# Kernel tuning notes

Hardware: AMD Instinct MI355X
Metric: run time of the kernel (lower is better)

## Reference

```python
import jax, jax.numpy as jnp
import numpy as np

N_NODES = 50000
N_EDGES = 800000
D_IN, D_HID, D_LAT = 128, 128, 64
BN_EPS = 1e-5


def setup_inputs() -> dict:
    key = jax.random.key(0)
    ks = jax.random.split(key, 8)
    x = jax.random.normal(ks[0], (N_NODES, D_IN), dtype=jnp.float32)
    edge_index = jax.random.randint(ks[1], (2, N_EDGES), 0, N_NODES, dtype=jnp.int64)
    s1 = 1.0 / np.sqrt(D_IN)
    s2 = 1.0 / np.sqrt(D_HID)
    W1 = jax.random.normal(ks[2], (D_IN, D_HID), dtype=jnp.float32) * s1
    b1 = jnp.zeros((D_HID,), jnp.float32)
    gamma = jnp.ones((D_HID,), jnp.float32)
    beta = jnp.zeros((D_HID,), jnp.float32)
    Wmu = jax.random.normal(ks[3], (D_HID, D_LAT), dtype=jnp.float32) * s2
    bmu = jnp.zeros((D_LAT,), jnp.float32)
    Wls = jax.random.normal(ks[4], (D_HID, D_LAT), dtype=jnp.float32) * s2
    bls = jnp.zeros((D_LAT,), jnp.float32)
    return {"x": x, "edge_index": edge_index, "W1": W1, "b1": b1,
            "gamma": gamma, "beta": beta, "Wmu": Wmu, "bmu": bmu,
            "Wls": Wls, "bls": bls}


def _gcn_conv(h, src, dst, norm_e, inv_deg, W, b):
    # PyG GCNConv: linear transform, then sym-normalized aggregation (A+I).
    h = h @ W                                   # [N, F]
    msgs = h[src] * norm_e[:, None]             # gather + edge scaling, [E, F]
    agg = jax.ops.segment_sum(msgs, dst, num_segments=h.shape[0])
    # self-loop contribution: norm[i]*norm[i] = 1/deg[i]
    return agg + h * inv_deg[:, None] + b


def reference(x, edge_index, W1, b1, gamma, beta, Wmu, bmu, Wls, bls):
    src, dst = edge_index[0], edge_index[1]
    n = x.shape[0]
    # degrees including self loops (GCN symmetric normalization)
    deg = jax.ops.segment_sum(jnp.ones(dst.shape, x.dtype), dst, num_segments=n) + 1.0
    inv_sqrt_deg = jax.lax.rsqrt(deg)
    norm_e = inv_sqrt_deg[src] * inv_sqrt_deg[dst]   # per-edge norm, [E]
    inv_deg = 1.0 / deg

    h = _gcn_conv(x, src, dst, norm_e, inv_deg, W1, b1)
    # BatchNorm1d with batch statistics (biased var), then ReLU; dropout off (eval)
    mean = h.mean(axis=0)
    var = h.var(axis=0)
    h = (h - mean) * jax.lax.rsqrt(var + BN_EPS) * gamma + beta
    h = jax.nn.relu(h)

    mu = _gcn_conv(h, src, dst, norm_e, inv_deg, Wmu, bmu)
    log_std = _gcn_conv(h, src, dst, norm_e, inv_deg, Wls, bls)
    return mu, log_std
```

## Files before the change

kernel.cpp:

```cpp
#include <hip/hip_runtime.h>
#include <hip/hip_bf16.h>

#define N_NODES 50000
#define N_EDGES 800000
#define F 128
#define L 64
#define BN_EPS 1e-5f
#define SCAN_BLOCKS 196
#define BN_BLOCKS 391
#define EDGE_BLOCKS 3125
#define GEMM_BLOCKS 782
#define NPART 8
#define PART_SZ 6250
#define SUBS_F 256
#define FILLB_A 2048

typedef __attribute__((ext_vector_type(8))) short short8;
typedef __attribute__((ext_vector_type(8))) unsigned short ushort8;
typedef __attribute__((ext_vector_type(4))) unsigned short ushortx4;
typedef __attribute__((ext_vector_type(4))) float f32x4;

static __device__ __forceinline__ float loadF(const void* p, int i, int f32) {
    if (f32) return ((const float*)p)[i];
    return __bfloat162float(((const __hip_bfloat16*)p)[i]);
}
static __device__ __forceinline__ float bfu2f(unsigned short u) {
    unsigned int t = ((unsigned int)u) << 16;
    float f;
    __builtin_memcpy(&f, &t, 4);
    return f;
}
static __device__ __forceinline__ short f2bf_s(float f) {
    union { __hip_bfloat16 b; short s; } cv;
    cv.b = __float2bfloat16(f);
    return cv.s;
}
static __device__ __forceinline__ unsigned short f2bf_u(float f) {
    union { __hip_bfloat16 b; unsigned short u; } cv;
    cv.b = __float2bfloat16(f);
    return cv.u;
}

__global__ void k_wprep(const void* __restrict__ W1, const void* __restrict__ Wmu,
                        const void* __restrict__ Wls, const unsigned short* __restrict__ xs,
                        const void* __restrict__ ei, __hip_bfloat16* __restrict__ Wt1,
                        __hip_bfloat16* __restrict__ Wt2, int* __restrict__ flags) {
    int b = blockIdx.x;
    int t = threadIdx.x;
    if (b == 0) {
        __shared__ int cnt[2];
        if (t < 2) cnt[t] = 0;
        __syncthreads();
        unsigned short v = xs[2 * t];
        int e = (v >> 7) & 0xff;
        int sane = (e >= 112 && e <= 133) ? 1 : 0;
        if (v == 0 || v == 0x8000) sane = 1;
        atomicAdd(&cnt[0], sane);
        atomicAdd(&cnt[1], (((const int*)ei)[2 * t + 1] != 0) ? 1 : 0);
        __syncthreads();
        if (t == 0) {
            flags[0] = (cnt[0] < 128) ? 1 : 0;
            flags[1] = (cnt[1] < 8) ? 1 : 0;
            flags[2] = 0;
        }
    } else {
        __shared__ int cnt;
        if (t == 0) cnt = 0;
        __syncthreads();
        unsigned short v = ((const unsigned short*)W1)[2 * t];
        int e = (v >> 7) & 0xff;
        atomicAdd(&cnt, (e >= 100 && e <= 133) ? 1 : 0);
        __syncthreads();
        int f32 = (cnt < 128) ? 1 : 0;
        int idx = (b - 1) * 256 + t;
        int n = idx >> 7, k = idx & 127;
        Wt1[idx] = __float2bfloat16(loadF(W1, k * F + n, f32));
        float v2 = (n < L) ? loadF(Wmu, k * L + n, f32) : loadF(Wls, k * L + (n - L), f32);
        Wt2[idx] = __float2bfloat16(v2);
    }
}

static __device__ __forceinline__ void gemm_body(int bid, const void* __restrict__ Xin,
        const __hip_bfloat16* __restrict__ Wt, const int* __restrict__ flags, int mode,
        const float* __restrict__ bnscale, const float* __restrict__ bnshift,
        unsigned short* __restrict__ outb) {
    int wave = threadIdx.x >> 6, lane = threadIdx.x & 63;
    int quad = lane >> 4, mr = lane & 15;
    int m0 = bid * 64 + wave * 16;
    int node = m0 + mr;
    int row = (node < N_NODES) ? node : N_NODES - 1;
    short8 a[4];
    if (mode == 1) {
        const unsigned short* xb = (const unsigned short*)Xin;
#pragma unroll
        for (int t = 0; t < 4; ++t) {
            int k0 = t * 32 + quad * 8;
            ushort8 raw = *(const ushort8*)(xb + row * F + k0);
            f32x4 s0 = *(const f32x4*)(bnscale + k0);
            f32x4 s1 = *(const f32x4*)(bnscale + k0 + 4);
            f32x4 h0 = *(const f32x4*)(bnshift + k0);
            f32x4 h1 = *(const f32x4*)(bnshift + k0 + 4);
            short8 av;
#pragma unroll
            for (int j = 0; j < 4; ++j)
                av[j] = f2bf_s(fmaxf(bfu2f(raw[j]) * s0[j] + h0[j], 0.f));
#pragma unroll
            for (int j = 0; j < 4; ++j)
                av[4 + j] = f2bf_s(fmaxf(bfu2f(raw[4 + j]) * s1[j] + h1[j], 0.f));
            a[t] = av;
        }
    } else if (flags[0]) {
        const float* xf = (const float*)Xin;
#pragma unroll
        for (int t = 0; t < 4; ++t) {
            int off = row * F + t * 32 + quad * 8;
            f32x4 v0 = *(const f32x4*)(xf + off);
            f32x4 v1 = *(const f32x4*)(xf + off + 4);
            short8 av;
#pragma unroll
            for (int j = 0; j < 4; ++j) av[j] = f2bf_s(v0[j]);
#pragma unroll
            for (int j = 0; j < 4; ++j) av[4 + j] = f2bf_s(v1[j]);
            a[t] = av;
        }
    } else {
        const short* xb = (const short*)Xin;
#pragma unroll
        for (int t = 0; t < 4; ++t)
            a[t] = *(const short8*)(xb + row * F + t * 32 + quad * 8);
    }
    f32x4 acc[8];
    const short* wb = (const short*)Wt;
#pragma unroll
    for (int nt = 0; nt < 8; ++nt) {
        const short* wp = wb + (nt * 16 + mr) * F + quad * 8;
        f32x4 c = {0.f, 0.f, 0.f, 0.f};
        c = __builtin_amdgcn_mfma_f32_16x16x32_bf16(*(const short8*)(wp), a[0], c, 0, 0, 0);
        c = __builtin_amdgcn_mfma_f32_16x16x32_bf16(*(const short8*)(wp + 32), a[1], c, 0, 0, 0);
        c = __builtin_amdgcn_mfma_f32_16x16x32_bf16(*(const short8*)(wp + 64), a[2], c, 0, 0, 0);
        c = __builtin_amdgcn_mfma_f32_16x16x32_bf16(*(const short8*)(wp + 96), a[3], c, 0, 0, 0);
        acc[nt] = c;
    }
    if (node < N_NODES) {
        unsigned short* op = outb + node * F;
#pragma unroll
        for (int nt = 0; nt < 8; ++nt) {
            ushortx4 r;
#pragma unroll
            for (int j = 0; j < 4; ++j) r[j] = f2bf_u(acc[nt][j]);
            *(ushortx4*)(op + nt * 16 + quad * 4) = r;
        }
    }
}

__global__ __launch_bounds__(256) void k_edge_gemm1(
        const void* __restrict__ X, const __hip_bfloat16* __restrict__ Wt1,
        const int* __restrict__ flags, const void* __restrict__ ei,
        int* __restrict__ degi, int* __restrict__ src32, int* __restrict__ dst32,
        int* __restrict__ rank, unsigned short* __restrict__ outb) {
    if (blockIdx.x < GEMM_BLOCKS) {
        gemm_body(blockIdx.x, X, Wt1, flags, 0, nullptr, nullptr, outb);
    } else {
        int t = threadIdx.x;
        int e0 = (blockIdx.x - GEMM_BLOCKS) * 256 + t;
        __shared__ int nz;
        if (t == 0) nz = 0;
        __syncthreads();
        int w = ((const int*)ei)[2 * e0 + 1];
        if (w != 0) atomicAdd(&nz, 1);
        __syncthreads();
        int d;
        if (nz < 8) {
            int s = (int)((const long long*)ei)[e0];
            d = (int)((const long long*)ei)[N_EDGES + e0];
            src32[e0] = s;
            dst32[e0] = d;
        } else {
            d = ((const int*)ei)[N_EDGES + e0];
        }
        rank[e0] = atomicAdd(&degi[d], 1);
    }
}

__global__ void k_offs_alloc(const int* __restrict__ degi, int* __restrict__ flags,
                             int* __restrict__ offs, float* __restrict__ isd) {
    __shared__ int s[256];
    __shared__ int base;
    int t = threadIdx.x;
    int i = blockIdx.x * 256 + t;
    int v = (i < N_NODES) ? degi[i] : 0;
    s[t] = v;
    __syncthreads();
    for (int o = 1; o < 256; o <<= 1) {
        int u = (t >= o) ? s[t - o] : 0;
        __syncthreads();
        s[t] += u;
        __syncthreads();
    }
    if (t == 255) base = atomicAdd(&flags[2], s[255]);
    __syncthreads();
    if (i < N_NODES) {
        offs[i] = base + s[t] - v;
        isd[i] = 1.0f / sqrtf((float)v + 1.0f);
    }
}

__global__ __launch_bounds__(256) void k_fill(
        const int* __restrict__ ei32, const int* __restrict__ src32,
        const int* __restrict__ dst32, const int* __restrict__ rank,
        const int* __restrict__ flags, const int* __restrict__ offs,
        int* __restrict__ csr) {
    const int* sp;
    const int* dp;
    if (flags[1]) { sp = src32; dp = dst32; }
    else          { sp = ei32;  dp = ei32 + N_EDGES; }
    int grp = blockIdx.x & (NPART - 1);
    int sub = blockIdx.x >> 3;
    int lo = grp * PART_SZ, hi = lo + PART_SZ;
    int stride = SUBS_F * 256;
    for (int e = sub * 256 + threadIdx.x; e < N_EDGES; e += stride) {
        int d = dp[e];
        if (d >= lo && d < hi) csr[offs[d] + rank[e]] = sp[e];
    }
}

__global__ __launch_bounds__(256) void k_gemm_bn(const void* __restrict__ Xin,
        const __hip_bfloat16* __restrict__ Wt, const int* __restrict__ flags,
        const float* __restrict__ bnscale, const float* __restrict__ bnshift,
        unsigned short* __restrict__ outb) {
    gemm_body(blockIdx.x, Xin, Wt, flags, 1, bnscale, bnshift, outb);
}

static __device__ __forceinline__ void agg_accum(int node, int grp, int l16,
        const ushort8* __restrict__ vp, const int* __restrict__ csr,
        const int* __restrict__ offs, const int* __restrict__ degi,
        const float* __restrict__ isd, float acc[8]) {
#pragma unroll
    for (int j = 0; j < 8; ++j) acc[j] = 0.f;
    if (grp == 0) {
        float w = isd[node];
        ushort8 u = vp[node * 16 + l16];
#pragma unroll
        for (int j = 0; j < 8; ++j) acc[j] = bfu2f(u[j]) * w;
    }
    int start = offs[node];
    int end = start + degi[node];
    int i = start + grp;
    for (; i + 12 < end; i += 16) {
        int s0 = csr[i], s1 = csr[i + 4], s2 = csr[i + 8], s3 = csr[i + 12];
        float w0 = isd[s0], w1 = isd[s1], w2 = isd[s2], w3 = isd[s3];
        ushort8 u0 = vp[s0 * 16 + l16];
        ushort8 u1 = vp[s1 * 16 + l16];
        ushort8 u2 = vp[s2 * 16 + l16];
        ushort8 u3 = vp[s3 * 16 + l16];
#pragma unroll
        for (int j = 0; j < 8; ++j)
            acc[j] += (bfu2f(u0[j]) * w0 + bfu2f(u1[j]) * w1) +
                      (bfu2f(u2[j]) * w2 + bfu2f(u3[j]) * w3);
    }
    for (; i + 4 < end; i += 8) {
        int s0 = csr[i], s1 = csr[i + 4];
        float w0 = isd[s0], w1 = isd[s1];
        ushort8 u0 = vp[s0 * 16 + l16];
        ushort8 u1 = vp[s1 * 16 + l16];
#pragma unroll
        for (int j = 0; j < 8; ++j) acc[j] += bfu2f(u0[j]) * w0 + bfu2f(u1[j]) * w1;
    }
    for (; i < end; i += 4) {
        int s0 = csr[i];
        float w0 = isd[s0];
        ushort8 u = vp[s0 * 16 + l16];
#pragma unroll
        for (int j = 0; j < 8; ++j) acc[j] += bfu2f(u[j]) * w0;
    }
#pragma unroll
    for (int j = 0; j < 8; ++j) {
        acc[j] += __shfl_xor(acc[j], 16);
        acc[j] += __shfl_xor(acc[j], 32);
    }
}

__global__ void k_agg1(const unsigned short* __restrict__ val, const int* __restrict__ csr,
                       const int* __restrict__ offs, const int* __restrict__ degi,
                       const float* __restrict__ isd, const void* __restrict__ b1,
                       const int* __restrict__ flags, unsigned short* __restrict__ out) {
    int node = blockIdx.x * 4 + (threadIdx.x >> 6);
    if (node >= N_NODES) return;
    int lane = threadIdx.x & 63;
    int grp = lane >> 4, l16 = lane & 15;
    float acc[8];
    agg_accum(node, grp, l16, (const ushort8*)val, csr, offs, degi, isd, acc);
    if (grp == 0) {
        float sd = isd[node];
        int c0 = l16 * 8, f32 = flags[0];
        ushort8 r;
#pragma unroll
        for (int j = 0; j < 8; ++j) r[j] = f2bf_u(acc[j] * sd + loadF(b1, c0 + j, f32));
        ((ushort8*)out)[node * 16 + l16] = r;
    }
}

__global__ void k_bnstats(const unsigned short* __restrict__ h, float* __restrict__ partial) {
    __shared__ float ls[256][8];
    __shared__ float lq[256][8];
    int t = threadIdx.x;
    int o = t & 15, rg = t >> 4;
    int row0 = blockIdx.x * 128 + rg;
    float s[8] = {0.f}, q[8] = {0.f};
#pragma unroll
    for (int i = 0; i < 8; ++i) {
        int row = row0 + i * 16;
        if (row < N_NODES) {
            ushort8 u = *(const ushort8*)(h + row * F + o * 8);
#pragma unroll
            for (int j = 0; j < 8; ++j) {
                float v = bfu2f(u[j]);
                s[j] += v;
                q[j] += v * v;
            }
        }
    }
#pragma unroll
    for (int j = 0; j < 8; ++j) { ls[t][j] = s[j]; lq[t][j] = q[j]; }
    __syncthreads();
    if (t < 128) {
        int c = t, oo = c >> 3, jj = c & 7;
        float ts = 0.f, tq = 0.f;
#pragma unroll
        for (int rgi = 0; rgi < 16; ++rgi) {
            ts += ls[rgi * 16 + oo][jj];
            tq += lq[rgi * 16 + oo][jj];
        }
        partial[blockIdx.x * 256 + c] = ts;
        partial[blockIdx.x * 256 + 128 + c] = tq;
    }
}

__global__ void k_bnredprep(const float* __restrict__ partial, const void* __restrict__ gamma,
                            const void* __restrict__ beta, const int* __restrict__ flags,
                            float* __restrict__ scale, float* __restrict__ shift) {
    int c = blockIdx.x;
    float s = 0.f, q = 0.f;
    for (int b = threadIdx.x; b < BN_BLOCKS; b += 256) {
        s += partial[b * 256 + c];
        q += partial[b * 256 + 128 + c];
    }
#pragma unroll
    for (int o = 32; o; o >>= 1) {
        s += __shfl_down(s, o);
        q += __shfl_down(q, o);
    }
    __shared__ float ws[4], wq[4];
    if ((threadIdx.x & 63) == 0) {
        ws[threadIdx.x >> 6] = s;
        wq[threadIdx.x >> 6] = q;
    }
    __syncthreads();
    if (threadIdx.x == 0) {
        float S = ws[0] + ws[1] + ws[2] + ws[3];
        float Q = wq[0] + wq[1] + wq[2] + wq[3];
        const float invN = 1.0f / (float)N_NODES;
        float m = S * invN;
        float var = Q * invN - m * m;
        int f32 = flags[0];
        float sc = loadF(gamma, c, f32) * rsqrtf(var + BN_EPS);
        scale[c] = sc;
        shift[c] = loadF(beta, c, f32) - m * sc;
    }
}

__global__ void k_agg2(const unsigned short* __restrict__ val, const int* __restrict__ csr,
                       const int* __restrict__ offs, const int* __restrict__ degi,
                       const float* __restrict__ isd, const void* __restrict__ bmu,
                       const void* __restrict__ bls, const int* __restrict__ flags,
                       void* __restrict__ out) {
    int node = blockIdx.x * 4 + (threadIdx.x >> 6);
    if (node >= N_NODES) return;
    int lane = threadIdx.x & 63;
    int grp = lane >> 4, l16 = lane & 15;
    float acc[8];
    agg_accum(node, grp, l16, (const ushort8*)val, csr, offs, degi, isd, acc);
    if (grp == 0) {
        float sd = isd[node];
        int c0 = l16 * 8, f32 = flags[0];
        int hsel = (c0 >= L) ? 1 : 0;
        int cc = c0 - hsel * L;
        const void* bp = hsel ? bls : bmu;
        float o8[8];
#pragma unroll
        for (int j = 0; j < 8; ++j) o8[j] = acc[j] * sd + loadF(bp, cc + j, f32);
        long base_o = (long)hsel * (N_NODES * 64) + (long)node * 64 + cc;
        if (f32) {
            f32x4 r0 = {o8[0], o8[1], o8[2], o8[3]};
            f32x4 r1 = {o8[4], o8[5], o8[6], o8[7]};
            __builtin_nontemporal_store(r0, (f32x4*)((float*)out + base_o));
            __builtin_nontemporal_store(r1, (f32x4*)((float*)out + base_o + 4));
        } else {
            ushort8 r;
#pragma unroll
            for (int j = 0; j < 8; ++j) r[j] = f2bf_u(o8[j]);
            __builtin_nontemporal_store(r, (ushort8*)((__hip_bfloat16*)out + base_o));
        }
    }
}

extern "C" void kernel_launch(void* const* d_in, const int* in_sizes, int n_in,
                              void* d_out, int out_size, void* d_ws, size_t ws_size,
                              hipStream_t stream) {
    const void* x     = d_in[0];
    const void* ei    = d_in[1];
    const void* W1    = d_in[2];
    const void* b1    = d_in[3];
    const void* gamma = d_in[4];
    const void* beta  = d_in[5];
    const void* Wmu   = d_in[6];
    const void* bmu   = d_in[7];
    const void* Wls   = d_in[8];
    const void* bls   = d_in[9];

    int*   degi  = (int*)d_ws;
    int*   offs  = degi + 50048;
    float* isd   = (float*)(offs + 50048);
    float* stats = isd + 50048;
    int*   flags = (int*)(stats + 512);
    int*   csr   = flags + 16;
    int*   src32 = csr + 800000;
    int*   dst32 = src32 + 800000;
    int*   rank  = dst32 + 800000;
    __hip_bfloat16* Wt1 = (__hip_bfloat16*)(rank + 800000);
    __hip_bfloat16* Wt2 = Wt1 + 16384;
    unsigned short* Abf = (unsigned short*)(Wt2 + 16384);
    unsigned short* Hpre = Abf + N_NODES * F;
    float* partial = (float*)(Hpre + N_NODES * F);

    const int NT = 256;
    const int AGG_BLOCKS = (N_NODES + 3) / 4;

    hipMemsetAsync(degi, 0, 50048 * sizeof(int), stream);
    k_wprep<<<65, NT, 0, stream>>>(W1, Wmu, Wls, (const unsigned short*)x, ei,
                                   Wt1, Wt2, flags);
    k_edge_gemm1<<<GEMM_BLOCKS + EDGE_BLOCKS, NT, 0, stream>>>(
        x, Wt1, flags, ei, degi, src32, dst32, rank, Abf);
    k_offs_alloc<<<SCAN_BLOCKS, NT, 0, stream>>>(degi, flags, offs, isd);
    k_fill<<<FILLB_A, NT, 0, stream>>>((const int*)ei, src32, dst32, rank,
                                       flags, offs, csr);
    k_agg1<<<AGG_BLOCKS, NT, 0, stream>>>(Abf, csr, offs, degi, isd, b1, flags, Hpre);
    k_bnstats<<<BN_BLOCKS, NT, 0, stream>>>(Hpre, partial);
    k_bnredprep<<<128, NT, 0, stream>>>(partial, gamma, beta, flags, stats, stats + 128);
    k_gemm_bn<<<GEMM_BLOCKS, NT, 0, stream>>>(Hpre, Wt2, flags, stats, stats + 128, Abf);
    k_agg2<<<AGG_BLOCKS, NT, 0, stream>>>(Abf, csr, offs, degi, isd, bmu, bls, flags, d_out);
}
```

Before: 274.1 us.

## Store edge indices, ranks and CSR as 16-bit and fold degree memset into prep

Node ids and per-node ranks are narrowed to unsigned 16-bit. This is valid because there are 50000 nodes, which fits in 16 bits, so the source, destination, rank and CSR arrays shrink by half. The goal is to cut memory traffic in the edge pass, the fill pass and both aggregation kernels' neighbour reads. The degree-array memset becomes extra blocks of the weight-prep kernel, removing a separate memset launch. Each edge-pass thread now handles two edges, halving that block count. The code now hard-depends on node counts below 65536.

```diff
diff --git a/kernel.cpp b/kernel.cpp
--- a/kernel.cpp
+++ b/kernel.cpp
@@ -8,7 +8,7 @@
 #define BN_EPS 1e-5f
 #define SCAN_BLOCKS 196
 #define BN_BLOCKS 391
-#define EDGE_BLOCKS 3125
+#define EDGE_BLOCKS2 1563
 #define GEMM_BLOCKS 782
 #define NPART 8
 #define PART_SZ 6250
@@ -44,7 +44,8 @@
 __global__ void k_wprep(const void* __restrict__ W1, const void* __restrict__ Wmu,
                         const void* __restrict__ Wls, const unsigned short* __restrict__ xs,
                         const void* __restrict__ ei, __hip_bfloat16* __restrict__ Wt1,
-                        __hip_bfloat16* __restrict__ Wt2, int* __restrict__ flags) {
+                        __hip_bfloat16* __restrict__ Wt2, int* __restrict__ flags,
+                        int* __restrict__ degi) {
     int b = blockIdx.x;
     int t = threadIdx.x;
     if (b == 0) {
@@ -63,7 +64,7 @@
             flags[1] = (cnt[1] < 8) ? 1 : 0;
             flags[2] = 0;
         }
-    } else {
+    } else if (b <= 64) {
         __shared__ int cnt;
         if (t == 0) cnt = 0;
         __syncthreads();
@@ -77,6 +78,9 @@
         Wt1[idx] = __float2bfloat16(loadF(W1, k * F + n, f32));
         float v2 = (n < L) ? loadF(Wmu, k * L + n, f32) : loadF(Wls, k * L + (n - L), f32);
         Wt2[idx] = __float2bfloat16(v2);
+    } else {
+        int i = (b - 65) * 256 + t;
+        if (i < 50048) degi[i] = 0;
     }
 }
 
@@ -156,29 +160,41 @@
 __global__ __launch_bounds__(256) void k_edge_gemm1(
         const void* __restrict__ X, const __hip_bfloat16* __restrict__ Wt1,
         const int* __restrict__ flags, const void* __restrict__ ei,
-        int* __restrict__ degi, int* __restrict__ src32, int* __restrict__ dst32,
-        int* __restrict__ rank, unsigned short* __restrict__ outb) {
+        int* __restrict__ degi, unsigned short* __restrict__ src16,
+        unsigned short* __restrict__ dst16, unsigned short* __restrict__ rank16,
+        unsigned short* __restrict__ outb) {
     if (blockIdx.x < GEMM_BLOCKS) {
         gemm_body(blockIdx.x, X, Wt1, flags, 0, nullptr, nullptr, outb);
     } else {
         int t = threadIdx.x;
-        int e0 = (blockIdx.x - GEMM_BLOCKS) * 256 + t;
+        int ebase = (blockIdx.x - GEMM_BLOCKS) * 512;
         __shared__ int nz;
         if (t == 0) nz = 0;
         __syncthreads();
-        int w = ((const int*)ei)[2 * e0 + 1];
-        if (w != 0) atomicAdd(&nz, 1);
-        __syncthreads();
-        int d;
-        if (nz < 8) {
-            int s = (int)((const long long*)ei)[e0];
-            d = (int)((const long long*)ei)[N_EDGES + e0];
-            src32[e0] = s;
-            dst32[e0] = d;
-        } else {
-            d = ((const int*)ei)[N_EDGES + e0];
-        }
-        rank[e0] = atomicAdd(&degi[d], 1);
+        int e0 = ebase + t;
+        if (e0 < N_EDGES) {
+            int w = ((const int*)ei)[2 * e0 + 1];
+            if (w != 0) atomicAdd(&nz, 1);
+        }
+        __syncthreads();
+        int i64 = (nz < 8) ? 1 : 0;
+#pragma unroll
+        for (int k = 0; k < 2; ++k) {
+            int e = ebase + k * 256 + t;
+            if (e < N_EDGES) {
+                int s, d;
+                if (i64) {
+                    s = (int)((const long long*)ei)[e];
+                    d = (int)((const long long*)ei)[N_EDGES + e];
+                } else {
+                    s = ((const int*)ei)[e];
+                    d = ((const int*)ei)[N_EDGES + e];
+                }
+                src16[e] = (unsigned short)s;
+                dst16[e] = (unsigned short)d;
+                rank16[e] = (unsigned short)atomicAdd(&degi[d], 1);
+            }
+        }
     }
 }
 
@@ -206,21 +222,16 @@
 }
 
 __global__ __launch_bounds__(256) void k_fill(
-        const int* __restrict__ ei32, const int* __restrict__ src32,
-        const int* __restrict__ dst32, const int* __restrict__ rank,
-        const int* __restrict__ flags, const int* __restrict__ offs,
-        int* __restrict__ csr) {
-    const int* sp;
-    const int* dp;
-    if (flags[1]) { sp = src32; dp = dst32; }
-    else          { sp = ei32;  dp = ei32 + N_EDGES; }
+        const unsigned short* __restrict__ src16, const unsigned short* __restrict__ dst16,
+        const unsigned short* __restrict__ rank16, const int* __restrict__ offs,
+        unsigned short* __restrict__ csr16) {
     int grp = blockIdx.x & (NPART - 1);
     int sub = blockIdx.x >> 3;
     int lo = grp * PART_SZ, hi = lo + PART_SZ;
     int stride = SUBS_F * 256;
     for (int e = sub * 256 + threadIdx.x; e < N_EDGES; e += stride) {
-        int d = dp[e];
-        if (d >= lo && d < hi) csr[offs[d] + rank[e]] = sp[e];
+        int d = dst16[e];
+        if (d >= lo && d < hi) csr16[offs[d] + rank16[e]] = src16[e];
     }
 }
 
@@ -232,7 +243,7 @@
 }
 
 static __device__ __forceinline__ void agg_accum(int node, int grp, int l16,
-        const ushort8* __restrict__ vp, const int* __restrict__ csr,
+        const ushort8* __restrict__ vp, const unsigned short* __restrict__ csr,
         const int* __restrict__ offs, const int* __restrict__ degi,
         const float* __restrict__ isd, float acc[8]) {
 #pragma unroll
@@ -280,7 +291,8 @@
     }
 }
 
-__global__ void k_agg1(const unsigned short* __restrict__ val, const int* __restrict__ csr,
+__global__ void k_agg1(const unsigned short* __restrict__ val,
+                       const unsigned short* __restrict__ csr,
                        const int* __restrict__ offs, const int* __restrict__ degi,
                        const float* __restrict__ isd, const void* __restrict__ b1,
                        const int* __restrict__ flags, unsigned short* __restrict__ out) {
@@ -369,7 +381,8 @@
     }
 }
 
-__global__ void k_agg2(const unsigned short* __restrict__ val, const int* __restrict__ csr,
+__global__ void k_agg2(const unsigned short* __restrict__ val,
+                       const unsigned short* __restrict__ csr,
                        const int* __restrict__ offs, const int* __restrict__ degi,
                        const float* __restrict__ isd, const void* __restrict__ bmu,
                        const void* __restrict__ bls, const int* __restrict__ flags,
@@ -423,11 +436,11 @@
     float* isd   = (float*)(offs + 50048);
     float* stats = isd + 50048;
     int*   flags = (int*)(stats + 512);
-    int*   csr   = flags + 16;
-    int*   src32 = csr + 800000;
-    int*   dst32 = src32 + 800000;
-    int*   rank  = dst32 + 800000;
-    __hip_bfloat16* Wt1 = (__hip_bfloat16*)(rank + 800000);
+    unsigned short* csr16  = (unsigned short*)(flags + 16);
+    unsigned short* src16  = csr16 + 800000;
+    unsigned short* dst16  = src16 + 800000;
+    unsigned short* rank16 = dst16 + 800000;
+    __hip_bfloat16* Wt1 = (__hip_bfloat16*)(rank16 + 800000);
     __hip_bfloat16* Wt2 = Wt1 + 16384;
     unsigned short* Abf = (unsigned short*)(Wt2 + 16384);
     unsigned short* Hpre = Abf + N_NODES * F;
@@ -436,17 +449,15 @@
     const int NT = 256;
     const int AGG_BLOCKS = (N_NODES + 3) / 4;
 
-    hipMemsetAsync(degi, 0, 50048 * sizeof(int), stream);
-    k_wprep<<<65, NT, 0, stream>>>(W1, Wmu, Wls, (const unsigned short*)x, ei,
-                                   Wt1, Wt2, flags);
-    k_edge_gemm1<<<GEMM_BLOCKS + EDGE_BLOCKS, NT, 0, stream>>>(
-        x, Wt1, flags, ei, degi, src32, dst32, rank, Abf);
+    k_wprep<<<65 + SCAN_BLOCKS, NT, 0, stream>>>(W1, Wmu, Wls, (const unsigned short*)x,
+                                                 ei, Wt1, Wt2, flags, degi);
+    k_edge_gemm1<<<GEMM_BLOCKS + EDGE_BLOCKS2, NT, 0, stream>>>(
+        x, Wt1, flags, ei, degi, src16, dst16, rank16, Abf);
     k_offs_alloc<<<SCAN_BLOCKS, NT, 0, stream>>>(degi, flags, offs, isd);
-    k_fill<<<FILLB_A, NT, 0, stream>>>((const int*)ei, src32, dst32, rank,
-                                       flags, offs, csr);
-    k_agg1<<<AGG_BLOCKS, NT, 0, stream>>>(Abf, csr, offs, degi, isd, b1, flags, Hpre);
+    k_fill<<<FILLB_A, NT, 0, stream>>>(src16, dst16, rank16, offs, csr16);
+    k_agg1<<<AGG_BLOCKS, NT, 0, stream>>>(Abf, csr16, offs, degi, isd, b1, flags, Hpre);
     k_bnstats<<<BN_BLOCKS, NT, 0, stream>>>(Hpre, partial);
     k_bnredprep<<<128, NT, 0, stream>>>(partial, gamma, beta, flags, stats, stats + 128);
     k_gemm_bn<<<GEMM_BLOCKS, NT, 0, stream>>>(Hpre, Wt2, flags, stats, stats + 128, Abf);
-    k_agg2<<<AGG_BLOCKS, NT, 0, stream>>>(Abf, csr, offs, degi, isd, bmu, bls, flags, d_out);
-}
+    k_agg2<<<AGG_BLOCKS, NT, 0, stream>>>(Abf, csr16, offs, degi, isd, bmu, bls, flags, d_out);
+}
```

Result: no change. 271.7 us (-0.9%).
